# Kernel optimization log

Hardware: AMD Instinct MI355X
Metric: run time of the kernel (lower is better)

The kernel has to match this reference:

```python
import jax, jax.numpy as jnp
import numpy as np

B, H, W, C = 16, 64, 64, 256
DIM = 256

def setup_inputs() -> dict:
    key = jax.random.key(0)
    ks = jax.random.split(key, 9)
    s_in = 1.0 / np.sqrt(C)
    x = jax.random.normal(ks[0], (B, H, W, C), dtype=jnp.float32)
    Wq = jax.random.normal(ks[1], (C, DIM), dtype=jnp.float32) * s_in
    bq = jnp.zeros((DIM,), dtype=jnp.float32)
    Wk = jax.random.normal(ks[2], (C, DIM), dtype=jnp.float32) * s_in
    bk = jnp.zeros((DIM,), dtype=jnp.float32)
    Wv = jax.random.normal(ks[3], (C, DIM), dtype=jnp.float32) * s_in
    bv = jnp.zeros((DIM,), dtype=jnp.float32)
    # 'out' conv sees 1 input channel (after the channel reduce_sum)
    Wo = jax.random.normal(ks[4], (1, DIM), dtype=jnp.float32)
    bo = jnp.zeros((DIM,), dtype=jnp.float32)
    return {"x": x, "Wq": Wq, "bq": bq, "Wk": Wk, "bk": bk,
            "Wv": Wv, "bv": bv, "Wo": Wo, "bo": bo}

def reference(x, Wq, bq, Wk, bk, Wv, bv, Wo, bo):
    # 1x1 convs == channel GEMMs
    q = jnp.einsum('bhwc,cd->bhwd', x, Wq) + bq
    k = jnp.einsum('bhwc,cd->bhwd', x, Wk) + bk
    v = jnp.einsum('bhwc,cd->bhwd', x, Wv) + bv
    # channel-reduce score -> [B,H,W,1], softmax jointly over spatial axes
    score = jnp.sum(q * k, axis=-1, keepdims=True)
    attn = jax.nn.softmax(score, axis=(1, 2))
    # channel-reduce of v weighted by per-pixel attn -> [B,H,W,1]
    out = jnp.sum(v * attn, axis=-1, keepdims=True)
    # final 1x1 conv: 1 input channel -> DIM output channels
    return jnp.einsum('bhwc,cd->bhwd', out, Wo) + bo
```

## Files before the change

kernel.cpp:

```cpp
#include <hip/hip_runtime.h>


typedef __bf16 bf16_t;
typedef __attribute__((ext_vector_type(8))) __bf16 bf16x8;
typedef __attribute__((ext_vector_type(4))) float f32x4;

#define NBATCH 16
#define NPIX   65536
#define PPB    4096

#define MH_OFF    0u
#define ML_OFF    131072u
#define U_OFF     262144u
#define WV_OFF    263168u
#define SCL_OFF   264192u
#define SCORE_OFF 264448u
#define SV_OFF    526592u
#define BMAX_OFF  788736u
#define BSUM_OFF  788800u

__global__ __launch_bounds__(256) void prep_kernel(
    const float* __restrict__ Wq, const float* __restrict__ bq,
    const float* __restrict__ Wk, const float* __restrict__ bk,
    const float* __restrict__ Wv, const float* __restrict__ bv,
    bf16_t* __restrict__ Mh, bf16_t* __restrict__ Ml,
    float* __restrict__ u, float* __restrict__ wv, float* __restrict__ scl)
{
    const int t = threadIdx.x;
    if (blockIdx.x < 256) {
        const int c = blockIdx.x;
        __shared__ __align__(16) float wq_row[256];
        wq_row[t] = Wq[c * 256 + t];
        __syncthreads();
        const float4* wk4 = (const float4*)(Wk + t * 256);
        const float4* wq4 = (const float4*)wq_row;
        float acc = 0.f;
#pragma unroll 8
        for (int i = 0; i < 64; ++i) {
            float4 a = wq4[i], b = wk4[i];
            acc += a.x * b.x + a.y * b.y + a.z * b.z + a.w * b.w;
        }
        bf16_t h = (bf16_t)acc;
        float hf = (float)h;
        bf16_t l = (bf16_t)(acc - hf);
        Mh[c * 256 + t] = h;
        Ml[c * 256 + t] = l;
    } else {
        float uacc = 0.f, wvacc = 0.f;
        const float* wqr = Wq + t * 256;
        const float* wkr = Wk + t * 256;
        const float* wvr = Wv + t * 256;
#pragma unroll 4
        for (int d = 0; d < 256; ++d) {
            uacc += wqr[d] * bk[d] + wkr[d] * bq[d];
            wvacc += wvr[d];
        }
        u[t] = uacc;
        wv[t] = wvacc;
        __shared__ float r1[256], r2[256];
        r1[t] = bq[t] * bk[t];
        r2[t] = bv[t];
        __syncthreads();
        for (int s = 128; s > 0; s >>= 1) {
            if (t < s) { r1[t] += r1[t + s]; r2[t] += r2[t + s]; }
            __syncthreads();
        }
        if (t == 0) { scl[0] = r1[0]; scl[1] = r2[0]; }
    }
}

__device__ __forceinline__ int swz(int row, int col) {
    return row * 256 + (col ^ ((row & 7) << 3));
}

__global__ __launch_bounds__(512, 2) void score_kernel(
    const float* __restrict__ x,
    const bf16_t* __restrict__ Mh, const bf16_t* __restrict__ Ml,
    const float* __restrict__ u, const float* __restrict__ wvp,
    const float* __restrict__ scl,
    float* __restrict__ score, float* __restrict__ svout)
{
    __shared__ __align__(16) char smem[65536];
    __shared__ float redS[8][64];
    __shared__ float svp[64], tpp[64];
    bf16_t* Ah = (bf16_t*)smem;
    bf16_t* Al = Ah + 16384;

    const int t = threadIdx.x;
    const int lane = t & 63;
    const int wid = t >> 6;
    const int l15 = lane & 15;
    const int lg = lane >> 4;
    const int wcol0 = wid * 32;

    const int srow = t >> 3;
    const int sch = (t & 7) * 16;

    bf16x8 Bh[8][2], Bl[8][2];
#pragma unroll
    for (int kk = 0; kk < 8; ++kk)
#pragma unroll
        for (int cf = 0; cf < 2; ++cf) {
            size_t bo = (size_t)(wcol0 + cf * 16 + l15) * 256 + kk * 32 + lg * 8;
            Bh[kk][cf] = *(const bf16x8*)(Mh + bo);
            Bl[kk][cf] = *(const bf16x8*)(Ml + bo);
        }

#define CVT_WRITE_DOTS(XV, H)                                                 \
    {                                                                         \
        _Pragma("unroll")                                                     \
        for (int j = 0; j < 2; ++j) {                                         \
            bf16x8 hi, lo;                                                    \
            _Pragma("unroll")                                                 \
            for (int e = 0; e < 8; ++e) {                                     \
                float f = ((const float*)XV)[j * 8 + e];                      \
                bf16_t h = (bf16_t)f;                                         \
                hi[e] = h;                                                    \
                lo[e] = (bf16_t)(f - (float)h);                               \
            }                                                                 \
            int idx = swz(srow, (H) * 128 + sch + j * 8);                     \
            *(bf16x8*)&Ah[idx] = hi;                                          \
            *(bf16x8*)&Al[idx] = lo;                                          \
        }                                                                     \
        _Pragma("unroll")                                                     \
        for (int i = 0; i < 4; ++i) {                                         \
            float4 wvv = *(const float4*)(wvp + (H) * 128 + sch + i * 4);     \
            float4 uvv = *(const float4*)(u + (H) * 128 + sch + i * 4);       \
            sv_acc += XV[i].x * wvv.x + XV[i].y * wvv.y +                     \
                      XV[i].z * wvv.z + XV[i].w * wvv.w;                      \
            tp_acc += XV[i].x * uvv.x + XV[i].y * uvv.y +                     \
                      XV[i].z * uvv.z + XV[i].w * uvv.w;                      \
        }                                                                     \
    }

#define MFMA_HALF(H)                                                          \
    _Pragma("unroll")                                                         \
    for (int ks = 0; ks < 4; ++ks) {                                          \
        const int kk = (H) * 4 + ks;                                          \
        const int k0 = kk * 32;                                               \
        bf16x8 afh[4], afl[4];                                                \
        _Pragma("unroll")                                                     \
        for (int rf = 0; rf < 4; ++rf) {                                      \
            int idx = swz(rf * 16 + l15, k0 + lg * 8);                        \
            afh[rf] = *(const bf16x8*)&Ah[idx];                               \
            afl[rf] = *(const bf16x8*)&Al[idx];                               \
        }                                                                     \
        _Pragma("unroll")                                                     \
        for (int rf = 0; rf < 4; ++rf)                                        \
            _Pragma("unroll")                                                 \
            for (int cf = 0; cf < 2; ++cf) {                                  \
                acc[rf][cf] = __builtin_amdgcn_mfma_f32_16x16x32_bf16(        \
                    afh[rf], Bh[kk][cf], acc[rf][cf], 0, 0, 0);               \
                acc[rf][cf] = __builtin_amdgcn_mfma_f32_16x16x32_bf16(        \
                    afl[rf], Bh[kk][cf], acc[rf][cf], 0, 0, 0);               \
                acc[rf][cf] = __builtin_amdgcn_mfma_f32_16x16x32_bf16(        \
                    afh[rf], Bl[kk][cf], acc[rf][cf], 0, 0, 0);               \
            }                                                                 \
    }

    float4 xva[4], xvb[4];
    {
        const float* xrow = x + (size_t)((size_t)blockIdx.x * 128 + srow) * 256;
#pragma unroll
        for (int i = 0; i < 4; ++i) xva[i] = *(const float4*)(xrow + sch + i * 4);
    }

#pragma unroll 2
    for (int tt = 0; tt < 2; ++tt) {
        const int pix0 = (blockIdx.x * 2 + tt) * 64;
        const float* xrow = x + (size_t)(pix0 + srow) * 256;
        float sv_acc = 0.f, tp_acc = 0.f;

        f32x4 acc[4][2];
#pragma unroll
        for (int i = 0; i < 4; ++i)
#pragma unroll
            for (int j = 0; j < 2; ++j)
                acc[i][j] = (f32x4){0.f, 0.f, 0.f, 0.f};

        CVT_WRITE_DOTS(xva, 0);
#pragma unroll
        for (int i = 0; i < 4; ++i) xvb[i] = *(const float4*)(xrow + 128 + sch + i * 4);

        __syncthreads();
        MFMA_HALF(0);

        CVT_WRITE_DOTS(xvb, 1);
        if (tt == 0) {
            const float* xrow2 = x + (size_t)(pix0 + 64 + srow) * 256;
#pragma unroll
            for (int i = 0; i < 4; ++i) xva[i] = *(const float4*)(xrow2 + sch + i * 4);
        }
#pragma unroll
        for (int m = 1; m < 8; m <<= 1) {
            sv_acc += __shfl_xor(sv_acc, m, 64);
            tp_acc += __shfl_xor(tp_acc, m, 64);
        }
        if ((lane & 7) == 0) { svp[srow] = sv_acc; tpp[srow] = tp_acc; }

        __syncthreads();
        MFMA_HALF(1);

        float sacc[4][4];
#pragma unroll
        for (int rf = 0; rf < 4; ++rf) {
#pragma unroll
            for (int r = 0; r < 4; ++r) {
                int row = rf * 16 + lg * 4 + r;
                float s = 0.f;
#pragma unroll
                for (int cf = 0; cf < 2; ++cf) {
                    int idx = swz(row, wcol0 + cf * 16 + l15);
                    float xv = (float)Ah[idx] + (float)Al[idx];
                    s += xv * acc[rf][cf][r];
                }
#pragma unroll
                for (int m = 1; m < 16; m <<= 1) s += __shfl_xor(s, m, 64);
                sacc[rf][r] = s;
            }
        }
        __syncthreads();
        if (l15 == 0) {
#pragma unroll
            for (int rf = 0; rf < 4; ++rf)
#pragma unroll
                for (int r = 0; r < 4; ++r)
                    redS[wid][rf * 16 + lg * 4 + r] = sacc[rf][r];
        }
        __syncthreads();
        if (t < 64) {
            float s = tpp[t] + scl[0];
#pragma unroll
            for (int w = 0; w < 8; ++w) s += redS[w][t];
            score[pix0 + t] = s;
            svout[pix0 + t] = svp[t] + scl[1];
        }
    }
#undef CVT_WRITE_DOTS
#undef MFMA_HALF
}

__global__ __launch_bounds__(256) void stats_kernel(
    const float* __restrict__ score,
    float* __restrict__ bmax, float* __restrict__ bsum)
{
    const int b = blockIdx.x, t = threadIdx.x;
    const int lane = t & 63, wid = t >> 6;
    const float4* s4 = (const float4*)(score + b * PPB);
    float4 v[4];
#pragma unroll
    for (int i = 0; i < 4; ++i) v[i] = s4[t + i * 256];
    float m = v[0].x;
#pragma unroll
    for (int i = 0; i < 4; ++i) {
        m = fmaxf(m, fmaxf(fmaxf(v[i].x, v[i].y), fmaxf(v[i].z, v[i].w)));
    }
    float sum = 0.f;
#pragma unroll
    for (int i = 0; i < 4; ++i) {
        sum += __expf(v[i].x - m) + __expf(v[i].y - m) +
               __expf(v[i].z - m) + __expf(v[i].w - m);
    }
#pragma unroll
    for (int k = 1; k < 64; k <<= 1) {
        float om = __shfl_xor(m, k, 64);
        float os = __shfl_xor(sum, k, 64);
        float nm = fmaxf(m, om);
        sum = sum * __expf(m - nm) + os * __expf(om - nm);
        m = nm;
    }
    __shared__ float sm[4], ss[4];
    if (lane == 0) { sm[wid] = m; ss[wid] = sum; }
    __syncthreads();
    if (t == 0) {
        float M = fmaxf(fmaxf(sm[0], sm[1]), fmaxf(sm[2], sm[3]));
        float S = ss[0] * __expf(sm[0] - M) + ss[1] * __expf(sm[1] - M) +
                  ss[2] * __expf(sm[2] - M) + ss[3] * __expf(sm[3] - M);
        bmax[b] = M; bsum[b] = S;
    }
}

__global__ __launch_bounds__(256) void out_kernel(
    const float* __restrict__ score, const float* __restrict__ sv,
    const float* __restrict__ bmax, const float* __restrict__ bsum,
    const float* __restrict__ Wo, const float* __restrict__ bo,
    float* __restrict__ out)
{
    const int total = NPIX * 64;
    const int stride = gridDim.x * blockDim.x;
    for (int idx = blockIdx.x * blockDim.x + threadIdx.x; idx < total; idx += stride) {
        int p = idx >> 6;
        int c4 = (idx & 63) << 2;
        int b = p >> 12;
        float g = __expf(score[p] - bmax[b]) / bsum[b] * sv[p];
        float4 w = *(const float4*)(Wo + c4);
        float4 bb = *(const float4*)(bo + c4);
        float4 o = { g * w.x + bb.x, g * w.y + bb.y, g * w.z + bb.z, g * w.w + bb.w };
        *(float4*)(out + (size_t)p * 256 + c4) = o;
    }
}

extern "C" void kernel_launch(void* const* d_in, const int* in_sizes, int n_in,
                              void* d_out, int out_size, void* d_ws, size_t ws_size,
                              hipStream_t stream) {
    const float* x  = (const float*)d_in[0];
    const float* Wq = (const float*)d_in[1];
    const float* bq = (const float*)d_in[2];
    const float* Wk = (const float*)d_in[3];
    const float* bk = (const float*)d_in[4];
    const float* Wv = (const float*)d_in[5];
    const float* bv = (const float*)d_in[6];
    const float* Wo = (const float*)d_in[7];
    const float* bo = (const float*)d_in[8];
    float* out = (float*)d_out;
    char* ws = (char*)d_ws;

    bf16_t* Mh = (bf16_t*)(ws + MH_OFF);
    bf16_t* Ml = (bf16_t*)(ws + ML_OFF);
    float* u   = (float*)(ws + U_OFF);
    float* wv  = (float*)(ws + WV_OFF);
    float* scl = (float*)(ws + SCL_OFF);
    float* score = (float*)(ws + SCORE_OFF);
    float* sv    = (float*)(ws + SV_OFF);
    float* bmax  = (float*)(ws + BMAX_OFF);
    float* bsum  = (float*)(ws + BSUM_OFF);

    prep_kernel<<<dim3(257), dim3(256), 0, stream>>>(Wq, bq, Wk, bk, Wv, bv, Mh, Ml, u, wv, scl);
    score_kernel<<<dim3(NPIX / 128), dim3(512), 0, stream>>>(x, Mh, Ml, u, wv, scl, score, sv);
    stats_kernel<<<dim3(NBATCH), dim3(256), 0, stream>>>(score, bmax, bsum);
    out_kernel<<<dim3(4096), dim3(256), 0, stream>>>(score, sv, bmax, bsum, Wo, bo, out);
}
```

Baseline: 115.1 us.

## Symmetrize Gram matrix and drop low-part x MFMA pass in score kernel

The prep kernel now builds the symmetrized M = (WqWk^T + WkWq^T)/2. Because x^T M x is unchanged by symmetrizing, the score kernel can compensate for bf16 rounding of x algebraically: it multiplies by 2x - bf16(x) in the epilogue, so the x low-part MFMA pass is no longer needed. This removes a third of the MFMAs and the low-part LDS buffer. It also moves B fragments from resident registers to per-k global loads, processes one 64-pixel tile per block with twice as many blocks, and uses DPP row reductions. The tradeoffs are extra global reads of x in the epilogue, more global B-fragment traffic, the loss of the two-tile prefetch pipeline, and a small precision change from dropping the lo*lo error term.

```diff
diff --git a/kernel.cpp b/kernel.cpp
--- a/kernel.cpp
+++ b/kernel.cpp
@@ -30,19 +30,25 @@
     if (blockIdx.x < 256) {
         const int c = blockIdx.x;
         __shared__ __align__(16) float wq_row[256];
+        __shared__ __align__(16) float wk_row[256];
         wq_row[t] = Wq[c * 256 + t];
+        wk_row[t] = Wk[c * 256 + t];
         __syncthreads();
-        const float4* wk4 = (const float4*)(Wk + t * 256);
+        const float4* wkt = (const float4*)(Wk + t * 256);
+        const float4* wqt = (const float4*)(Wq + t * 256);
         const float4* wq4 = (const float4*)wq_row;
-        float acc = 0.f;
+        const float4* wk4 = (const float4*)wk_row;
+        float d1 = 0.f, d2 = 0.f;
 #pragma unroll 8
         for (int i = 0; i < 64; ++i) {
-            float4 a = wq4[i], b = wk4[i];
-            acc += a.x * b.x + a.y * b.y + a.z * b.z + a.w * b.w;
-        }
-        bf16_t h = (bf16_t)acc;
-        float hf = (float)h;
-        bf16_t l = (bf16_t)(acc - hf);
+            float4 a = wq4[i], b = wkt[i];
+            d1 += a.x * b.x + a.y * b.y + a.z * b.z + a.w * b.w;
+            float4 e = wk4[i], f = wqt[i];
+            d2 += e.x * f.x + e.y * f.y + e.z * f.z + e.w * f.w;
+        }
+        float m = 0.5f * (d1 + d2);
+        bf16_t h = (bf16_t)m;
+        bf16_t l = (bf16_t)(m - (float)h);
         Mh[c * 256 + t] = h;
         Ml[c * 256 + t] = l;
     } else {
@@ -73,6 +79,14 @@
     return row * 256 + (col ^ ((row & 7) << 3));
 }
 
+__device__ __forceinline__ float rowsum16(float v) {
+    v += __int_as_float(__builtin_amdgcn_update_dpp(0, __float_as_int(v), 0x118, 0xF, 0xF, true));
+    v += __int_as_float(__builtin_amdgcn_update_dpp(0, __float_as_int(v), 0x114, 0xF, 0xF, true));
+    v += __int_as_float(__builtin_amdgcn_update_dpp(0, __float_as_int(v), 0x112, 0xF, 0xF, true));
+    v += __int_as_float(__builtin_amdgcn_update_dpp(0, __float_as_int(v), 0x111, 0xF, 0xF, true));
+    return v;
+}
+
 __global__ __launch_bounds__(512, 2) void score_kernel(
     const float* __restrict__ x,
     const bf16_t* __restrict__ Mh, const bf16_t* __restrict__ Ml,
@@ -80,164 +94,106 @@
     const float* __restrict__ scl,
     float* __restrict__ score, float* __restrict__ svout)
 {
-    __shared__ __align__(16) char smem[65536];
+    __shared__ __align__(16) bf16_t Ah[64 * 256];
     __shared__ float redS[8][64];
     __shared__ float svp[64], tpp[64];
-    bf16_t* Ah = (bf16_t*)smem;
-    bf16_t* Al = Ah + 16384;
 
     const int t = threadIdx.x;
     const int lane = t & 63;
     const int wid = t >> 6;
     const int l15 = lane & 15;
     const int lg = lane >> 4;
+    const int pix0 = blockIdx.x * 64;
     const int wcol0 = wid * 32;
 
     const int srow = t >> 3;
-    const int sch = (t & 7) * 16;
-
-    bf16x8 Bh[8][2], Bl[8][2];
-#pragma unroll
-    for (int kk = 0; kk < 8; ++kk)
+    const int sch = (t & 7) * 32;
+    const float* xrow = x + (size_t)(pix0 + srow) * 256 + sch;
+
+    float4 xv[8];
+#pragma unroll
+    for (int i = 0; i < 8; ++i) xv[i] = *(const float4*)(xrow + i * 4);
+#pragma unroll
+    for (int j = 0; j < 4; ++j) {
+        bf16x8 hi;
+#pragma unroll
+        for (int e = 0; e < 8; ++e) hi[e] = (bf16_t)(((const float*)xv)[j * 8 + e]);
+        *(bf16x8*)&Ah[swz(srow, sch + j * 8)] = hi;
+    }
+    float sv_acc = 0.f, tp_acc = 0.f;
+#pragma unroll
+    for (int i = 0; i < 8; ++i) {
+        float4 wvv = *(const float4*)(wvp + sch + i * 4);
+        float4 uvv = *(const float4*)(u + sch + i * 4);
+        sv_acc += xv[i].x * wvv.x + xv[i].y * wvv.y + xv[i].z * wvv.z + xv[i].w * wvv.w;
+        tp_acc += xv[i].x * uvv.x + xv[i].y * uvv.y + xv[i].z * uvv.z + xv[i].w * uvv.w;
+    }
+#pragma unroll
+    for (int m = 1; m < 8; m <<= 1) {
+        sv_acc += __shfl_xor(sv_acc, m, 64);
+        tp_acc += __shfl_xor(tp_acc, m, 64);
+    }
+    if ((t & 7) == 0) { svp[srow] = sv_acc; tpp[srow] = tp_acc; }
+
+    f32x4 acc[4][2];
+#pragma unroll
+    for (int i = 0; i < 4; ++i)
+#pragma unroll
+        for (int j = 0; j < 2; ++j)
+            acc[i][j] = (f32x4){0.f, 0.f, 0.f, 0.f};
+
+    __syncthreads();
+
+    const int bbase = (wcol0 + l15) * 256 + lg * 8;
+#pragma unroll
+    for (int ks = 0; ks < 8; ++ks) {
+        const int k0 = ks * 32;
+        bf16x8 af[4];
+#pragma unroll
+        for (int rf = 0; rf < 4; ++rf)
+            af[rf] = *(const bf16x8*)&Ah[swz(rf * 16 + l15, k0 + lg * 8)];
+        bf16x8 bh[2], bl[2];
 #pragma unroll
         for (int cf = 0; cf < 2; ++cf) {
-            size_t bo = (size_t)(wcol0 + cf * 16 + l15) * 256 + kk * 32 + lg * 8;
-            Bh[kk][cf] = *(const bf16x8*)(Mh + bo);
-            Bl[kk][cf] = *(const bf16x8*)(Ml + bo);
-        }
-
-#define CVT_WRITE_DOTS(XV, H)                                                 \
-    {                                                                         \
-        _Pragma("unroll")                                                     \
-        for (int j = 0; j < 2; ++j) {                                         \
-            bf16x8 hi, lo;                                                    \
-            _Pragma("unroll")                                                 \
-            for (int e = 0; e < 8; ++e) {                                     \
-                float f = ((const float*)XV)[j * 8 + e];                      \
-                bf16_t h = (bf16_t)f;                                         \
-                hi[e] = h;                                                    \
-                lo[e] = (bf16_t)(f - (float)h);                               \
-            }                                                                 \
-            int idx = swz(srow, (H) * 128 + sch + j * 8);                     \
-            *(bf16x8*)&Ah[idx] = hi;                                          \
-            *(bf16x8*)&Al[idx] = lo;                                          \
-        }                                                                     \
-        _Pragma("unroll")                                                     \
-        for (int i = 0; i < 4; ++i) {                                         \
-            float4 wvv = *(const float4*)(wvp + (H) * 128 + sch + i * 4);     \
-            float4 uvv = *(const float4*)(u + (H) * 128 + sch + i * 4);       \
-            sv_acc += XV[i].x * wvv.x + XV[i].y * wvv.y +                     \
-                      XV[i].z * wvv.z + XV[i].w * wvv.w;                      \
-            tp_acc += XV[i].x * uvv.x + XV[i].y * uvv.y +                     \
-                      XV[i].z * uvv.z + XV[i].w * uvv.w;                      \
-        }                                                                     \
-    }
-
-#define MFMA_HALF(H)                                                          \
-    _Pragma("unroll")                                                         \
-    for (int ks = 0; ks < 4; ++ks) {                                          \
-        const int kk = (H) * 4 + ks;                                          \
-        const int k0 = kk * 32;                                               \
-        bf16x8 afh[4], afl[4];                                                \
-        _Pragma("unroll")                                                     \
-        for (int rf = 0; rf < 4; ++rf) {                                      \
-            int idx = swz(rf * 16 + l15, k0 + lg * 8);                        \
-            afh[rf] = *(const bf16x8*)&Ah[idx];                               \
-            afl[rf] = *(const bf16x8*)&Al[idx];                               \
-        }                                                                     \
-        _Pragma("unroll")                                                     \
-        for (int rf = 0; rf < 4; ++rf)                                        \
-            _Pragma("unroll")                                                 \
-            for (int cf = 0; cf < 2; ++cf) {                                  \
-                acc[rf][cf] = __builtin_amdgcn_mfma_f32_16x16x32_bf16(        \
-                    afh[rf], Bh[kk][cf], acc[rf][cf], 0, 0, 0);               \
-                acc[rf][cf] = __builtin_amdgcn_mfma_f32_16x16x32_bf16(        \
-                    afl[rf], Bh[kk][cf], acc[rf][cf], 0, 0, 0);               \
-                acc[rf][cf] = __builtin_amdgcn_mfma_f32_16x16x32_bf16(        \
-                    afh[rf], Bl[kk][cf], acc[rf][cf], 0, 0, 0);               \
-            }                                                                 \
-    }
-
-    float4 xva[4], xvb[4];
-    {
-        const float* xrow = x + (size_t)((size_t)blockIdx.x * 128 + srow) * 256;
-#pragma unroll
-        for (int i = 0; i < 4; ++i) xva[i] = *(const float4*)(xrow + sch + i * 4);
-    }
-
-#pragma unroll 2
-    for (int tt = 0; tt < 2; ++tt) {
-        const int pix0 = (blockIdx.x * 2 + tt) * 64;
-        const float* xrow = x + (size_t)(pix0 + srow) * 256;
-        float sv_acc = 0.f, tp_acc = 0.f;
-
-        f32x4 acc[4][2];
-#pragma unroll
-        for (int i = 0; i < 4; ++i)
-#pragma unroll
-            for (int j = 0; j < 2; ++j)
-                acc[i][j] = (f32x4){0.f, 0.f, 0.f, 0.f};
-
-        CVT_WRITE_DOTS(xva, 0);
-#pragma unroll
-        for (int i = 0; i < 4; ++i) xvb[i] = *(const float4*)(xrow + 128 + sch + i * 4);
-
-        __syncthreads();
-        MFMA_HALF(0);
-
-        CVT_WRITE_DOTS(xvb, 1);
-        if (tt == 0) {
-            const float* xrow2 = x + (size_t)(pix0 + 64 + srow) * 256;
-#pragma unroll
-            for (int i = 0; i < 4; ++i) xva[i] = *(const float4*)(xrow2 + sch + i * 4);
-        }
-#pragma unroll
-        for (int m = 1; m < 8; m <<= 1) {
-            sv_acc += __shfl_xor(sv_acc, m, 64);
-            tp_acc += __shfl_xor(tp_acc, m, 64);
-        }
-        if ((lane & 7) == 0) { svp[srow] = sv_acc; tpp[srow] = tp_acc; }
-
-        __syncthreads();
-        MFMA_HALF(1);
-
-        float sacc[4][4];
-#pragma unroll
-        for (int rf = 0; rf < 4; ++rf) {
-#pragma unroll
-            for (int r = 0; r < 4; ++r) {
-                int row = rf * 16 + lg * 4 + r;
-                float s = 0.f;
-#pragma unroll
-                for (int cf = 0; cf < 2; ++cf) {
-                    int idx = swz(row, wcol0 + cf * 16 + l15);
-                    float xv = (float)Ah[idx] + (float)Al[idx];
-                    s += xv * acc[rf][cf][r];
-                }
-#pragma unroll
-                for (int m = 1; m < 16; m <<= 1) s += __shfl_xor(s, m, 64);
-                sacc[rf][r] = s;
+            bh[cf] = *(const bf16x8*)(Mh + bbase + cf * 4096 + k0);
+            bl[cf] = *(const bf16x8*)(Ml + bbase + cf * 4096 + k0);
+        }
+#pragma unroll
+        for (int rf = 0; rf < 4; ++rf)
+#pragma unroll
+            for (int cf = 0; cf < 2; ++cf) {
+                acc[rf][cf] = __builtin_amdgcn_mfma_f32_16x16x32_bf16(
+                    af[rf], bh[cf], acc[rf][cf], 0, 0, 0);
+                acc[rf][cf] = __builtin_amdgcn_mfma_f32_16x16x32_bf16(
+                    af[rf], bl[cf], acc[rf][cf], 0, 0, 0);
             }
-        }
-        __syncthreads();
-        if (l15 == 0) {
-#pragma unroll
-            for (int rf = 0; rf < 4; ++rf)
-#pragma unroll
-                for (int r = 0; r < 4; ++r)
-                    redS[wid][rf * 16 + lg * 4 + r] = sacc[rf][r];
-        }
-        __syncthreads();
-        if (t < 64) {
-            float s = tpp[t] + scl[0];
-#pragma unroll
-            for (int w = 0; w < 8; ++w) s += redS[w][t];
-            score[pix0 + t] = s;
-            svout[pix0 + t] = svp[t] + scl[1];
-        }
-    }
-#undef CVT_WRITE_DOTS
-#undef MFMA_HALF
+    }
+
+#pragma unroll
+    for (int rf = 0; rf < 4; ++rf) {
+#pragma unroll
+        for (int r = 0; r < 4; ++r) {
+            int row = rf * 16 + lg * 4 + r;
+            const float* xr = x + (size_t)(pix0 + row) * 256 + wcol0 + l15;
+            float s = 0.f;
+#pragma unroll
+            for (int cf = 0; cf < 2; ++cf) {
+                float xf = xr[cf * 16];
+                float e2 = 2.f * xf - (float)(bf16_t)xf;
+                s += e2 * acc[rf][cf][r];
+            }
+            s = rowsum16(s);
+            if (l15 == 15) redS[wid][row] = s;
+        }
+    }
+    __syncthreads();
+    if (t < 64) {
+        float s = tpp[t] + scl[0];
+#pragma unroll
+        for (int w = 0; w < 8; ++w) s += redS[w][t];
+        score[pix0 + t] = s;
+        svout[pix0 + t] = svp[t] + scl[1];
+    }
 }
 
 __global__ __launch_bounds__(256) void stats_kernel(
@@ -326,7 +282,7 @@
     float* bsum  = (float*)(ws + BSUM_OFF);
 
     prep_kernel<<<dim3(257), dim3(256), 0, stream>>>(Wq, bq, Wk, bk, Wv, bv, Mh, Ml, u, wv, scl);
-    score_kernel<<<dim3(NPIX / 128), dim3(512), 0, stream>>>(x, Mh, Ml, u, wv, scl, score, sv);
+    score_kernel<<<dim3(NPIX / 64), dim3(512), 0, stream>>>(x, Mh, Ml, u, wv, scl, score, sv);
     stats_kernel<<<dim3(NBATCH), dim3(256), 0, stream>>>(score, bmax, bsum);
     out_kernel<<<dim3(4096), dim3(256), 0, stream>>>(score, sv, bmax, bsum, Wo, bo, out);
 }
```

New measurement: 124.9 us, median of 2. 8.5% more time.
